# Kernel optimization log

Measured on AMD Instinct MI355X. Metric: run time of the kernel, lower is better.

## Reference

```python
import jax, jax.numpy as jnp
import numpy as np

B, S = 1, 2048
HID, INTER = 4096, 11008
HEADS, HD = 32, 128
GS = 128
EPS = 1e-6
BASE = 10000.0
IMIN, IMAX = -(2**31), 2**31 - 1


def _rope_tables():
    inv_freq = 1.0 / (BASE ** (np.arange(0, HD, 2, dtype=np.float32) / HD))
    t = np.arange(S, dtype=np.float32)
    freqs = np.outer(t, inv_freq)            # [S, HD/2]
    emb = np.concatenate([freqs, freqs], -1)  # [S, HD]
    return jnp.asarray(np.sin(emb), jnp.float32), jnp.asarray(np.cos(emb), jnp.float32)


def setup_inputs() -> dict:
    key = jax.random.key(0)
    ks = iter(jax.random.split(key, 40))
    def qset(in_f, out_f):
        qw = jax.random.randint(next(ks), (in_f // 8, out_f), IMIN, IMAX, dtype=jnp.int32)
        qz = jax.random.randint(next(ks), (in_f // GS, out_f // 8), IMIN, IMAX, dtype=jnp.int32)
        sc = jax.random.uniform(next(ks), (in_f // GS, out_f), dtype=jnp.float32) * 0.01 + 1e-3
        return qw, qz, sc
    dims = {"q": (HID, HID), "k": (HID, HID), "v": (HID, HID), "o": (HID, HID),
            "gate": (HID, INTER), "up": (HID, INTER), "down": (INTER, HID)}
    inp = {}
    for name, (i, o) in dims.items():
        qw, qz, sc = qset(i, o)
        inp["qw_" + name] = qw
        inp["qz_" + name] = qz
        inp["sc_" + name] = sc
    inp["hidden_states"] = jax.random.normal(next(ks), (B, S, HID), dtype=jnp.float32)
    inp["ln1_w"] = jnp.ones((HID,), jnp.float32)
    inp["ln2_w"] = jnp.ones((HID,), jnp.float32)
    sin, cos = _rope_tables()
    inp["sin"] = sin
    inp["cos"] = cos
    # causal additive mask, as stored in ExLlamaBuffer.attn_mask (past_len = 0)
    mask = jnp.where(jnp.tril(jnp.ones((S, S), bool)), 0.0, -1e9).astype(jnp.float32)
    inp["attn_mask"] = mask[None, None]
    return inp


def _dequant(qw, qz, sc):
    # GPTQ int4: qweight [in/8, out] packs 8 rows per int32; qzeros [groups, out/8]
    in_f, out_f = qw.shape[0] * 8, qw.shape[1]
    groups = sc.shape[0]
    sh = jnp.arange(8, dtype=jnp.int32) * 4
    w = ((qw[:, None, :] >> sh[None, :, None]) & 15)
    w = w.reshape(groups, in_f // groups, out_f).astype(jnp.float32)
    z = ((qz[:, :, None] >> sh[None, None, :]) & 15).reshape(groups, out_f).astype(jnp.float32)
    return ((w - (z + 1.0)[:, None, :]) * sc[:, None, :]).reshape(in_f, out_f)


def _rms(x, w):
    v = jnp.mean(x * x, axis=-1, keepdims=True)
    return x * jax.lax.rsqrt(v + EPS) * w


def _rot_half(x):
    x1, x2 = jnp.split(x, 2, axis=-1)
    return jnp.concatenate([-x2, x1], axis=-1)


def reference(qw_q, qz_q, sc_q, qw_k, qz_k, sc_k, qw_v, qz_v, sc_v,
              qw_o, qz_o, sc_o, qw_gate, qz_gate, sc_gate,
              qw_up, qz_up, sc_up, qw_down, qz_down, sc_down,
              hidden_states, ln1_w, ln2_w, sin, cos, attn_mask):
    lin = lambda x, a, b, c: x @ _dequant(a, b, c)
    h = hidden_states
    # attention block
    x = _rms(h, ln1_w)
    q = lin(x, qw_q, qz_q, sc_q).reshape(B, S, HEADS, HD).transpose(0, 2, 1, 3)
    k = lin(x, qw_k, qz_k, sc_k).reshape(B, S, HEADS, HD).transpose(0, 2, 1, 3)
    v = lin(x, qw_v, qz_v, sc_v).reshape(B, S, HEADS, HD).transpose(0, 2, 1, 3)
    c, s = cos[None, None], sin[None, None]  # [1,1,S,HD]
    q = q * c + _rot_half(q) * s
    k = k * c + _rot_half(k) * s
    scores = jnp.einsum('bhqd,bhkd->bhqk', q, k) / np.float32(np.sqrt(HD)) + attn_mask
    p = jax.nn.softmax(scores, axis=-1)
    o = jnp.einsum('bhqk,bhkd->bhqd', p, v).transpose(0, 2, 1, 3).reshape(B, S, HID)
    h = h + lin(o, qw_o, qz_o, sc_o)
    # MLP block
    x = _rms(h, ln2_w)
    y = jax.nn.silu(lin(x, qw_gate, qz_gate, sc_gate)) * lin(x, qw_up, qz_up, sc_up)
    return h + lin(y, qw_down, qz_down, sc_down)
```

## Files before the change

### kernel.cpp

```cpp
#include <hip/hip_runtime.h>
#include <cstdint>
#include <cstddef>

#define S_LEN 2048
#define HID   4096
#define INTER 11008
#define NHEADS 32
#define HD    128

typedef __attribute__((ext_vector_type(4))) float  f32x4;
typedef __attribute__((ext_vector_type(8))) __bf16 bf16x8;
typedef __attribute__((ext_vector_type(8))) short  s16x8;
typedef __attribute__((ext_vector_type(4))) short  s16x4;

__device__ __forceinline__ float bf2f(short s) {
  unsigned u = ((unsigned)(unsigned short)s) << 16;
  return __builtin_bit_cast(float, u);
}
__device__ __forceinline__ short f2bf(float f) {
  unsigned u = __builtin_bit_cast(unsigned, f);
  u += 0x7FFFu + ((u >> 16) & 1u);
  return (short)(u >> 16);
}
__device__ __forceinline__ f32x4 mfma16(s16x8 a, s16x8 b, f32x4 c) {
  return __builtin_amdgcn_mfma_f32_16x16x32_bf16(
      __builtin_bit_cast(bf16x8, a), __builtin_bit_cast(bf16x8, b), c, 0, 0, 0);
}
__device__ __forceinline__ void gload_lds16(const void* g, void* l) {
  __builtin_amdgcn_global_load_lds(
      (const __attribute__((address_space(1))) void*)g,
      (__attribute__((address_space(3))) void*)l, 16, 0, 0);
}

__global__ __launch_bounds__(256) void rmsnorm_kernel(const float* __restrict__ x,
                                                      const float* __restrict__ w,
                                                      short* __restrict__ out) {
  int row = blockIdx.x;
  const float* xr = x + (size_t)row * HID;
  short* orow = out + (size_t)row * HID;
  int tid = threadIdx.x;
  f32x4 v[4];
  float ss = 0.f;
#pragma unroll
  for (int i = 0; i < 4; ++i) {
    v[i] = ((const f32x4*)xr)[i * 256 + tid];
    ss += v[i][0] * v[i][0] + v[i][1] * v[i][1] + v[i][2] * v[i][2] + v[i][3] * v[i][3];
  }
#pragma unroll
  for (int off = 32; off > 0; off >>= 1) ss += __shfl_xor(ss, off);
  __shared__ float psum[4];
  if ((tid & 63) == 0) psum[tid >> 6] = ss;
  __syncthreads();
  float tot = psum[0] + psum[1] + psum[2] + psum[3];
  float r = rsqrtf(tot * (1.0f / (float)HID) + 1e-6f);
#pragma unroll
  for (int i = 0; i < 4; ++i) {
    int base = (i * 256 + tid) * 4;
    s16x4 o;
#pragma unroll
    for (int j = 0; j < 4; ++j) o[j] = f2bf(v[i][j] * r * w[base + j]);
    *(s16x4*)&orow[base] = o;
  }
}

__global__ __launch_bounds__(256) void dequant_kernel(const int* __restrict__ qw,
                                                      const int* __restrict__ qz,
                                                      const float* __restrict__ sc,
                                                      short* __restrict__ wt,
                                                      int N, int noff, int Kext) {
  __shared__ short tile[64 * 72];
  int n0 = blockIdx.x * 64;
  int k0 = blockIdx.y * 64;
  int g = k0 >> 7;
  int qr0 = k0 >> 3;
  int t = threadIdx.x;
#pragma unroll
  for (int i = 0; i < 2; ++i) {
    int idx = t + i * 256;
    int r = idx >> 6;
    int n = idx & 63;
    int gc = noff + n0 + n;
    unsigned q = (unsigned)qw[(size_t)(qr0 + r) * N + gc];
    float s = sc[(size_t)g * N + gc];
    unsigned zq = (unsigned)qz[(size_t)g * (N >> 3) + (gc >> 3)];
    float zs = ((float)((zq >> ((gc & 7) * 4)) & 15u) + 1.0f) * s;
    s16x8 o;
#pragma unroll
    for (int j = 0; j < 8; ++j)
      o[j] = f2bf(fmaf((float)((q >> (4 * j)) & 15u), s, -zs));
    *(s16x8*)&tile[n * 72 + r * 8] = o;
  }
  __syncthreads();
  int n = t >> 2;
#pragma unroll
  for (int i = 0; i < 2; ++i) {
    int c = (t & 3) + i * 4;
    *(s16x8*)&wt[(size_t)(n0 + n) * Kext + k0 + c * 8] = *(const s16x8*)&tile[n * 72 + c * 8];
  }
}

template <int OMODE>
__global__ __launch_bounds__(256) void gemm_kernel(const short* __restrict__ A, int lda,
                                                   const short* __restrict__ BT, int ldb,
                                                   void* __restrict__ Cv, int ldc,
                                                   const float* __restrict__ base,
                                                   int Kext) {
  __shared__ short As[2][128 * 32];
  __shared__ short Bs[2][128 * 32];
  int bn = blockIdx.x, bm = blockIdx.y;
  int tid = threadIdx.x;
  int lane = tid & 63, wv = tid >> 6;
  int wr = wv >> 1, wc = wv & 1;
  f32x4 acc[4][4] = {};
  int nk = Kext >> 5;
  int lr = lane >> 2;
  int lc = lane & 3;
  const short* Abase = A + (size_t)(bm * 128) * lda;
  const short* Bbase = BT + (size_t)(bn * 128) * ldb;

  auto stage = [&](int buf, int t) {
    int k0 = t << 5;
#pragma unroll
    for (int i = 0; i < 2; ++i) {
      int r = i * 64 + wv * 16 + lr;
      gload_lds16(Abase + (size_t)r * lda + k0 + lc * 8, &As[buf][i * 2048 + wv * 512]);
      gload_lds16(Bbase + (size_t)r * ldb + k0 + lc * 8, &Bs[buf][i * 2048 + wv * 512]);
    }
  };
  auto compute = [&](int buf) {
    int kc = (lane >> 4) * 8;
    int ra = wr * 64 + (lane & 15);
    int rb = wc * 64 + (lane & 15);
    s16x8 af[4], bfr[4];
#pragma unroll
    for (int m = 0; m < 4; ++m) af[m] = *(const s16x8*)&As[buf][(ra + m * 16) * 32 + kc];
#pragma unroll
    for (int n = 0; n < 4; ++n) bfr[n] = *(const s16x8*)&Bs[buf][(rb + n * 16) * 32 + kc];
#pragma unroll
    for (int m = 0; m < 4; ++m)
#pragma unroll
      for (int n = 0; n < 4; ++n) acc[m][n] = mfma16(af[m], bfr[n], acc[m][n]);
  };

  stage(0, 0);
  __syncthreads();
  for (int t = 0; t < nk; ++t) {
    if (t + 1 < nk) stage((t + 1) & 1, t + 1);
    compute(t & 1);
    __syncthreads();
  }

  int row0 = bm * 128 + wr * 64 + ((lane >> 4) << 2);
  int col0 = bn * 128 + wc * 64 + (lane & 15);
#pragma unroll
  for (int m = 0; m < 4; ++m)
#pragma unroll
    for (int n = 0; n < 4; ++n)
#pragma unroll
      for (int j = 0; j < 4; ++j) {
        size_t idx = (size_t)(row0 + m * 16 + j) * ldc + col0 + n * 16;
        if (OMODE == 0)      ((short*)Cv)[idx] = f2bf(acc[m][n][j]);
        else if (OMODE == 1) ((float*)Cv)[idx] = base[idx] + acc[m][n][j];
        else                 ((float*)Cv)[idx] = ((float*)Cv)[idx] + acc[m][n][j];
      }
}

__global__ __launch_bounds__(128) void rope_kernel(short* __restrict__ q, short* __restrict__ k,
                                                   const float* __restrict__ sp,
                                                   const float* __restrict__ cp) {
  int s = blockIdx.x, h = blockIdx.y;
  short* p = (blockIdx.z ? k : q) + (size_t)s * HID + h * HD;
  int d = threadIdx.x;
  float x = bf2f(p[d]);
  float xp = bf2f(p[d ^ 64]);
  float rot = (d < 64) ? -xp : xp;
  float y = x * cp[s * HD + d] + rot * sp[s * HD + d];
  __syncthreads();
  p[d] = f2bf(y);
}

__global__ __launch_bounds__(256) void attn_kernel(const short* __restrict__ qb,
                                                   const short* __restrict__ kb,
                                                   const short* __restrict__ vb,
                                                   short* __restrict__ ob) {
  int qt = (int)(gridDim.x - 1) - blockIdx.x;
  int h = blockIdx.y;
  int tid = threadIdx.x, lane = tid & 63, wv = tid >> 6;
  __shared__ short Kl[64 * 128];
  __shared__ short Vl[128 * 72];
  __shared__ short Pl[4][32 * 72];
  int q0 = qt * 128 + wv * 32;
  s16x8 qf[2][4];
#pragma unroll
  for (int m = 0; m < 2; ++m)
#pragma unroll
    for (int kf = 0; kf < 4; ++kf) {
      int r = q0 + m * 16 + (lane & 15);
      int d = kf * 32 + (lane >> 4) * 8;
      qf[m][kf] = *(const s16x8*)&qb[(size_t)r * HID + h * HD + d];
    }
  f32x4 o[2][8] = {};
  float mrow[2][4], lrow[2][4];
#pragma unroll
  for (int m = 0; m < 2; ++m)
#pragma unroll
    for (int j = 0; j < 4; ++j) { mrow[m][j] = -1e30f; lrow[m][j] = 0.f; }

  const float scale = 0.08838834764831845f;
  int kv_end = qt * 128 + 128;
  for (int kv0 = 0; kv0 < kv_end; kv0 += 64) {
    __syncthreads();
#pragma unroll
    for (int i = 0; i < 4; ++i) {
      int cid = tid + i * 256;
      int kv = cid >> 4, c = cid & 15;
      s16x8 kx = *(const s16x8*)(kb + (size_t)(kv0 + kv) * HID + h * HD + c * 8);
      *(s16x8*)((char*)Kl + kv * 256 + ((c ^ (kv & 7)) * 16)) = kx;
      s16x8 vx = *(const s16x8*)(vb + (size_t)(kv0 + kv) * HID + h * HD + c * 8);
      int kvs = kv ^ ((c & 7) << 3);
#pragma unroll
      for (int j = 0; j < 8; ++j) Vl[(c * 8 + j) * 72 + kvs] = vx[j];
    }
    __syncthreads();

    f32x4 sfr[2][4] = {};
    __builtin_amdgcn_s_setprio(1);
#pragma unroll
    for (int nf = 0; nf < 4; ++nf) {
      s16x8 kfr[4];
      int kvr = nf * 16 + (lane & 15);
#pragma unroll
      for (int kf = 0; kf < 4; ++kf) {
        int cc = (kf * 4 + (lane >> 4)) ^ (kvr & 7);
        kfr[kf] = *(const s16x8*)((const char*)Kl + kvr * 256 + cc * 16);
      }
#pragma unroll
      for (int m = 0; m < 2; ++m)
#pragma unroll
        for (int kf = 0; kf < 4; ++kf) sfr[m][nf] = mfma16(qf[m][kf], kfr[kf], sfr[m][nf]);
    }
    __builtin_amdgcn_s_setprio(0);
#pragma unroll
    for (int m = 0; m < 2; ++m)
#pragma unroll
      for (int j = 0; j < 4; ++j) {
        int qrow = q0 + m * 16 + (lane >> 4) * 4 + j;
        float pm = -1e30f;
#pragma unroll
        for (int nf = 0; nf < 4; ++nf) {
          int kvc = kv0 + nf * 16 + (lane & 15);
          float v = sfr[m][nf][j] * scale;
          v = (kvc <= qrow) ? v : -1e30f;
          sfr[m][nf][j] = v;
          pm = fmaxf(pm, v);
        }
#pragma unroll
        for (int off = 1; off < 16; off <<= 1) pm = fmaxf(pm, __shfl_xor(pm, off));
        float mnew = fmaxf(mrow[m][j], pm);
        float alpha = __expf(mrow[m][j] - mnew);
        mrow[m][j] = mnew;
        float rs = 0.f;
#pragma unroll
        for (int nf = 0; nf < 4; ++nf) {
          float p = __expf(sfr[m][nf][j] - mnew);
          sfr[m][nf][j] = p;
          rs += p;
        }
#pragma unroll
        for (int off = 1; off < 16; off <<= 1) rs += __shfl_xor(rs, off);
        lrow[m][j] = lrow[m][j] * alpha + rs;
#pragma unroll
        for (int nd = 0; nd < 8; ++nd) o[m][nd][j] *= alpha;
      }
#pragma unroll
    for (int m = 0; m < 2; ++m)
#pragma unroll
      for (int nf = 0; nf < 4; ++nf)
#pragma unroll
        for (int j = 0; j < 4; ++j)
          Pl[wv][(m * 16 + (lane >> 4) * 4 + j) * 72 + nf * 16 + (lane & 15)] =
              f2bf(sfr[m][nf][j]);
    s16x8 pa[2][2];
#pragma unroll
    for (int m = 0; m < 2; ++m)
#pragma unroll
      for (int kf = 0; kf < 2; ++kf)
        pa[m][kf] = *(const s16x8*)&Pl[wv][(m * 16 + (lane & 15)) * 72 + kf * 32 + (lane >> 4) * 8];
    __builtin_amdgcn_s_setprio(1);
#pragma unroll
    for (int nd = 0; nd < 8; ++nd) {
      s16x8 vf[2];
      int drow = nd * 16 + (lane & 15);
      int key = ((drow >> 3) & 7) << 3;
#pragma unroll
      for (int kf = 0; kf < 2; ++kf)
        vf[kf] = *(const s16x8*)&Vl[drow * 72 + ((kf * 32 + (lane >> 4) * 8) ^ key)];
#pragma unroll
      for (int m = 0; m < 2; ++m)
#pragma unroll
        for (int kf = 0; kf < 2; ++kf) o[m][nd] = mfma16(pa[m][kf], vf[kf], o[m][nd]);
    }
    __builtin_amdgcn_s_setprio(0);
  }
#pragma unroll
  for (int m = 0; m < 2; ++m)
#pragma unroll
    for (int nd = 0; nd < 8; ++nd)
#pragma unroll
      for (int j = 0; j < 4; ++j) {
        int r = q0 + m * 16 + (lane >> 4) * 4 + j;
        int c = h * HD + nd * 16 + (lane & 15);
        ob[(size_t)r * HID + c] = f2bf(o[m][nd][j] / lrow[m][j]);
      }
}

__global__ __launch_bounds__(256) void silumul_kernel(const short* __restrict__ g,
                                                      const short* __restrict__ u,
                                                      short* __restrict__ y) {
  size_t idx = (size_t)blockIdx.x * 256 + threadIdx.x;
  s16x8 gv = ((const s16x8*)g)[idx];
  s16x8 uv = ((const s16x8*)u)[idx];
  s16x8 yv;
#pragma unroll
  for (int j = 0; j < 8; ++j) {
    float gf = bf2f(gv[j]);
    float uf = bf2f(uv[j]);
    float sl = gf / (1.f + __expf(-gf));
    yv[j] = f2bf(sl * uf);
  }
  ((s16x8*)y)[idx] = yv;
}

extern "C" void kernel_launch(void* const* d_in, const int* in_sizes, int n_in,
                              void* d_out, int out_size, void* d_ws, size_t ws_size,
                              hipStream_t stream) {
  const int* qw[7]; const int* qz[7]; const float* sc[7];
  for (int i = 0; i < 7; ++i) {
    qw[i] = (const int*)d_in[i * 3 + 0];
    qz[i] = (const int*)d_in[i * 3 + 1];
    sc[i] = (const float*)d_in[i * 3 + 2];
  }
  const float* hin  = (const float*)d_in[21];
  const float* ln1  = (const float*)d_in[22];
  const float* ln2  = (const float*)d_in[23];
  const float* sinp = (const float*)d_in[24];
  const float* cosp = (const float*)d_in[25];
  float* out = (float*)d_out;

  char* ws = (char*)d_ws;
  const size_t MB = 1024 * 1024;
  short* XB    = (short*)(ws);
  short* WDQ   = (short*)(ws + 16 * MB);
  short* QB    = (short*)(ws + 48 * MB);
  short* KB    = (short*)(ws + 64 * MB);
  short* VB    = (short*)(ws + 80 * MB);
  short* OB    = (short*)(ws + 96 * MB);
  short* GATEB = (short*)(ws + 48 * MB);
  short* UPB   = (short*)(ws + 91 * MB);

  dim3 blk(256);
  dim3 dq44(64, 64);
  dim3 gm_hid(HID / 128, S_LEN / 128);

  rmsnorm_kernel<<<S_LEN, blk, 0, stream>>>(hin, ln1, XB);
  short* qkv_out[3] = {QB, KB, VB};
  for (int i = 0; i < 3; ++i) {
    dequant_kernel<<<dq44, blk, 0, stream>>>(qw[i], qz[i], sc[i], WDQ, HID, 0, HID);
    gemm_kernel<0><<<gm_hid, blk, 0, stream>>>(XB, HID, WDQ, HID, qkv_out[i], HID, nullptr, HID);
  }
  rope_kernel<<<dim3(S_LEN, NHEADS, 2), dim3(128), 0, stream>>>(QB, KB, sinp, cosp);
  attn_kernel<<<dim3(S_LEN / 128, NHEADS), blk, 0, stream>>>(QB, KB, VB, OB);
  dequant_kernel<<<dq44, blk, 0, stream>>>(qw[3], qz[3], sc[3], WDQ, HID, 0, HID);
  gemm_kernel<1><<<gm_hid, blk, 0, stream>>>(OB, HID, WDQ, HID, out, HID, hin, HID);
  rmsnorm_kernel<<<S_LEN, blk, 0, stream>>>(out, ln2, XB);
  const int noffs[3] = {0, 4096, 8192};
  const int nexts[3] = {4096, 4096, 2816};
  for (int c = 0; c < 3; ++c) {
    dequant_kernel<<<dim3(nexts[c] / 64, 64), blk, 0, stream>>>(qw[4], qz[4], sc[4], WDQ, INTER, noffs[c], HID);
    gemm_kernel<0><<<dim3(nexts[c] / 128, 16), blk, 0, stream>>>(XB, HID, WDQ, HID, GATEB + noffs[c], INTER, nullptr, HID);
  }
  for (int c = 0; c < 3; ++c) {
    dequant_kernel<<<dim3(nexts[c] / 64, 64), blk, 0, stream>>>(qw[5], qz[5], sc[5], WDQ, INTER, noffs[c], HID);
    gemm_kernel<0><<<dim3(nexts[c] / 128, 16), blk, 0, stream>>>(XB, HID, WDQ, HID, UPB + noffs[c], INTER, nullptr, HID);
  }
  silumul_kernel<<<(S_LEN * (size_t)INTER) / 8 / 256, blk, 0, stream>>>(GATEB, UPB, GATEB);
  for (int c = 0; c < 3; ++c) {
    int koff = noffs[c], kx = nexts[c];
    dequant_kernel<<<dim3(64, kx / 64), blk, 0, stream>>>(
        qw[6] + (size_t)(koff >> 3) * HID, qz[6] + (size_t)(koff >> 7) * (HID / 8),
        sc[6] + (size_t)(koff >> 7) * HID, WDQ, HID, 0, kx);
    gemm_kernel<2><<<gm_hid, blk, 0, stream>>>(GATEB + koff, INTER, WDQ, kx, out, HID, nullptr, kx);
  }
}
```

Before: 1.610 ms.

## Prefetch next KV tile into registers in attention and swizzle GEMM block order

The attention kernel now loads the next K/V tile from global memory into registers before computing on the current tile, then writes it to LDS after compute, so the global load latency is hidden behind the MFMA work. The GEMM kernel remaps block indices with a stride-8 swizzle to change the order in which tiles are scheduled, aiming at better cache locality across XCDs. Attention launch bounds now request two blocks per CU. The prefetch adds 32 VGPRs of staging registers, which together with the occupancy hint may cause spills.

```diff
diff --git a/kernel.cpp b/kernel.cpp
--- a/kernel.cpp
+++ b/kernel.cpp
@@ -107,7 +107,11 @@
                                                    int Kext) {
   __shared__ short As[2][128 * 32];
   __shared__ short Bs[2][128 * 32];
-  int bn = blockIdx.x, bm = blockIdx.y;
+  int nwg = gridDim.x * gridDim.y;
+  int lid = blockIdx.y * gridDim.x + blockIdx.x;
+  int cpx = nwg >> 3;
+  int swz = (lid & 7) * cpx + (lid >> 3);
+  int bn = swz % gridDim.x, bm = swz / gridDim.x;
   int tid = threadIdx.x;
   int lane = tid & 63, wv = tid >> 6;
   int wr = wv >> 1, wc = wv & 1;
@@ -179,10 +183,10 @@
   p[d] = f2bf(y);
 }
 
-__global__ __launch_bounds__(256) void attn_kernel(const short* __restrict__ qb,
-                                                   const short* __restrict__ kb,
-                                                   const short* __restrict__ vb,
-                                                   short* __restrict__ ob) {
+__global__ __launch_bounds__(256, 2) void attn_kernel(const short* __restrict__ qb,
+                                                      const short* __restrict__ kb,
+                                                      const short* __restrict__ vb,
+                                                      short* __restrict__ ob) {
   int qt = (int)(gridDim.x - 1) - blockIdx.x;
   int h = blockIdx.y;
   int tid = threadIdx.x, lane = tid & 63, wv = tid >> 6;
@@ -206,22 +210,36 @@
 #pragma unroll
     for (int j = 0; j < 4; ++j) { mrow[m][j] = -1e30f; lrow[m][j] = 0.f; }
 
-  const float scale = 0.08838834764831845f;
-  int kv_end = qt * 128 + 128;
-  for (int kv0 = 0; kv0 < kv_end; kv0 += 64) {
-    __syncthreads();
+  auto load_tile = [&](int kv0, s16x8* kr, s16x8* vr) {
 #pragma unroll
     for (int i = 0; i < 4; ++i) {
       int cid = tid + i * 256;
       int kv = cid >> 4, c = cid & 15;
-      s16x8 kx = *(const s16x8*)(kb + (size_t)(kv0 + kv) * HID + h * HD + c * 8);
-      *(s16x8*)((char*)Kl + kv * 256 + ((c ^ (kv & 7)) * 16)) = kx;
-      s16x8 vx = *(const s16x8*)(vb + (size_t)(kv0 + kv) * HID + h * HD + c * 8);
+      kr[i] = *(const s16x8*)(kb + (size_t)(kv0 + kv) * HID + h * HD + c * 8);
+      vr[i] = *(const s16x8*)(vb + (size_t)(kv0 + kv) * HID + h * HD + c * 8);
+    }
+  };
+  auto store_tile = [&](const s16x8* kr, const s16x8* vr) {
+#pragma unroll
+    for (int i = 0; i < 4; ++i) {
+      int cid = tid + i * 256;
+      int kv = cid >> 4, c = cid & 15;
+      *(s16x8*)((char*)Kl + kv * 256 + ((c ^ (kv & 7)) * 16)) = kr[i];
       int kvs = kv ^ ((c & 7) << 3);
 #pragma unroll
-      for (int j = 0; j < 8; ++j) Vl[(c * 8 + j) * 72 + kvs] = vx[j];
-    }
-    __syncthreads();
+      for (int j = 0; j < 8; ++j) Vl[(c * 8 + j) * 72 + kvs] = vr[i][j];
+    }
+  };
+
+  const float scale = 0.08838834764831845f;
+  int kv_end = qt * 128 + 128;
+  s16x8 kra[4], vra[4], krb[4], vrb[4];
+  load_tile(0, kra, vra);
+  store_tile(kra, vra);
+  __syncthreads();
+  for (int kv0 = 0; kv0 < kv_end; kv0 += 64) {
+    bool more = kv0 + 64 < kv_end;
+    if (more) load_tile(kv0 + 64, krb, vrb);
 
     f32x4 sfr[2][4] = {};
     __builtin_amdgcn_s_setprio(1);
@@ -301,6 +319,9 @@
         for (int kf = 0; kf < 2; ++kf) o[m][nd] = mfma16(pa[m][kf], vf[kf], o[m][nd]);
     }
     __builtin_amdgcn_s_setprio(0);
+    __syncthreads();
+    if (more) store_tile(krb, vrb);
+    __syncthreads();
   }
 #pragma unroll
   for (int m = 0; m < 2; ++m)
```

Result: no change. 1.582 ms (-1.7%).
